# Performance work log

Hardware: AMD Instinct MI355X
Metric: run time of the kernel (lower is better)

Reference implementation:

```python
import jax, jax.numpy as jnp
import numpy as np

# distilled LLaVA-style decoder: nf4-quantized linears + LoRA(q/k/v/o) + gumbel-softmax -> embedding einsum
B, S, D, H, L = 1, 2048, 2048, 16, 2
DH = D // H
DFF, V, R, BLK = 8192, 32000, 8, 64
LORA_SCALE = 16.0 / R  # alpha / r
TAU = 1.0
SQRT_DH = float(np.sqrt(DH))

# bitsandbytes NF4 codebook (16 values)
NF4 = jnp.array([-1.0, -0.6961928009986877, -0.5250730514526367, -0.39491748809814453,
                 -0.28444138169288635, -0.18477343022823334, -0.09105003625154495, 0.0,
                 0.07958029955625534, 0.16093020141124725, 0.24611230194568634,
                 0.33791524171829224, 0.44070982933044434, 0.5626170039176941,
                 0.7229568362236023, 1.0], dtype=jnp.float32)


def dequant(idx, scale):
    # idx [..., out, in] int in [0,16); scale [..., out, in//BLK] per-block absmax
    return NF4[idx] * jnp.repeat(scale, BLK, axis=-1)


def rmsnorm(x, w):
    return x * jax.lax.rsqrt(jnp.mean(x * x, axis=-1, keepdims=True) + 1e-6) * w


def setup_inputs():
    key = jax.random.key(0)
    k = jax.random.split(key, 12)
    return {
        "input_ids": jax.random.randint(k[0], (B, S), 0, V, dtype=jnp.int32),
        "u": jax.random.uniform(k[1], (B, S, V), dtype=jnp.float32),
        "emb": jax.random.normal(k[2], (V, D), dtype=jnp.float32) * 0.02,
        "attn_scale": jax.random.uniform(k[3], (L, 4, D, D // BLK), minval=0.005, maxval=0.02, dtype=jnp.float32),
        "ffn_gu_scale": jax.random.uniform(k[4], (L, 2, DFF, D // BLK), minval=0.005, maxval=0.02, dtype=jnp.float32),
        "ffn_d_scale": jax.random.uniform(k[5], (L, D, DFF // BLK), minval=0.005, maxval=0.02, dtype=jnp.float32),
        "lora_A": jax.random.normal(k[6], (L, 4, R, D), dtype=jnp.float32) * 0.01,
        "lora_B": jax.random.normal(k[7], (L, 4, D, R), dtype=jnp.float32) * 0.01,
        "norm_w": jnp.ones((L, 2, D), dtype=jnp.float32),
        "final_norm_w": jnp.ones((D,), dtype=jnp.float32),
        "attn_idx": jax.random.randint(k[8], (L, 4, D, D), 0, 16, dtype=jnp.int32),
        "ffn_gu_idx": jax.random.randint(k[9], (L, 2, DFF, D), 0, 16, dtype=jnp.int32),
        "ffn_d_idx": jax.random.randint(k[10], (L, D, DFF), 0, 16, dtype=jnp.int32),
    }


def reference(input_ids, u, emb, attn_scale, ffn_gu_scale, ffn_d_scale,
              lora_A, lora_B, norm_w, final_norm_w, attn_idx, ffn_gu_idx, ffn_d_idx):
    h = emb[input_ids]  # [B, S, D]
    causal = jnp.tril(jnp.ones((S, S), dtype=bool))
    for l in range(L):
        x = rmsnorm(h, norm_w[l, 0])
        w = dequant(attn_idx[l], attn_scale[l])  # [4, D, D] dequantized q/k/v/o weights

        def proj(i, t):
            # nf4 linear + LoRA adapter (y = t W^T + (t A^T) B^T * alpha/r)
            return t @ w[i].T + ((t @ lora_A[l, i].T) @ lora_B[l, i].T) * LORA_SCALE

        q = proj(0, x).reshape(B, S, H, DH)
        k_ = proj(1, x).reshape(B, S, H, DH)
        v = proj(2, x).reshape(B, S, H, DH)
        scores = jnp.einsum('bqhd,bkhd->bhqk', q, k_) / SQRT_DH
        scores = jnp.where(causal, scores, -1e30)
        p = jax.nn.softmax(scores, axis=-1)
        o = jnp.einsum('bhqk,bkhd->bqhd', p, v).reshape(B, S, D)
        h = h + proj(3, o)

        x = rmsnorm(h, norm_w[l, 1])
        wgu = dequant(ffn_gu_idx[l], ffn_gu_scale[l])  # [2, DFF, D] gate/up
        wd = dequant(ffn_d_idx[l], ffn_d_scale[l])     # [D, DFF] down
        h = h + (jax.nn.silu(x @ wgu[0].T) * (x @ wgu[1].T)) @ wd.T

    h = rmsnorm(h, final_norm_w)
    logits = h @ emb.T  # [B, S, V]
    # gumbel_softmax(tau, hard=False): softmax((logits + G)/tau), G = -log(-log(U))
    gnoise = -jnp.log(-jnp.log(u + 1e-10) + 1e-10)
    g = jax.nn.softmax((logits + gnoise) / TAU, axis=-1)
    soft_embeddings = jnp.einsum('bsv,vd->bsd', g, emb)
    return soft_embeddings, logits
```

## Files before the change

kernel.cpp:

```cpp
#include <hip/hip_runtime.h>
#include <hip/hip_bf16.h>

typedef unsigned short u16;
typedef unsigned int u32;
typedef __bf16 bf16t;
typedef bf16t bf16x8 __attribute__((ext_vector_type(8)));
typedef float f32x4 __attribute__((ext_vector_type(4)));

constexpr int S_   = 2048;
constexpr int D_   = 2048;
constexpr int H_   = 16;
constexpr int DH_  = 128;
constexpr int L_   = 2;
constexpr int DFF_ = 8192;
constexpr int V_   = 32000;
constexpr int R_   = 8;

#define MFMA16(a, b, c) __builtin_amdgcn_mfma_f32_16x16x32_bf16(a, b, c, 0, 0, 0)

__constant__ float c_nf4[16] = {
  -1.0f, -0.6961928009986877f, -0.5250730514526367f, -0.39491748809814453f,
  -0.28444138169288635f, -0.18477343022823334f, -0.09105003625154495f, 0.0f,
  0.07958029955625534f, 0.16093020141124725f, 0.24611230194568634f,
  0.33791524171829224f, 0.44070982933044434f, 0.5626170039176941f,
  0.7229568362236023f, 1.0f };

__device__ __forceinline__ u16 f2bf(float f) {
  union { float f; u32 u; } v; v.f = f;
  u32 r = v.u + 0x7fffu + ((v.u >> 16) & 1u);
  return (u16)(r >> 16);
}
__device__ __forceinline__ float bf2f(u16 h) {
  union { u32 u; float f; } v; v.u = ((u32)h) << 16; return v.f;
}

__global__ __launch_bounds__(256) void k_gather(const int* __restrict__ ids,
                                                const float* __restrict__ emb,
                                                float* __restrict__ h) {
  int t = blockIdx.x * 256 + threadIdx.x;
  int s = t >> 11;
  int d = t & 2047;
  h[t] = emb[(size_t)ids[s] * D_ + d];
}

__global__ __launch_bounds__(256) void k_rmsnorm(const float* __restrict__ in,
                                                 const float* __restrict__ w,
                                                 u16* __restrict__ out) {
  int s = blockIdx.x;
  const float* x = in + (size_t)s * D_;
  float ss = 0.f;
  for (int d = threadIdx.x; d < D_; d += 256) { float v = x[d]; ss += v * v; }
#pragma unroll
  for (int m = 1; m < 64; m <<= 1) ss += __shfl_xor(ss, m, 64);
  __shared__ float sh[4];
  if ((threadIdx.x & 63) == 0) sh[threadIdx.x >> 6] = ss;
  __syncthreads();
  ss = sh[0] + sh[1] + sh[2] + sh[3];
  float sc = rsqrtf(ss * (1.0f / D_) + 1e-6f);
  u16* o = out + (size_t)s * D_;
  for (int d = threadIdx.x; d < D_; d += 256) o[d] = f2bf(x[d] * sc * w[d]);
}

__global__ __launch_bounds__(256) void k_dequant(const int* __restrict__ idx,
                                                 const float* __restrict__ scale,
                                                 u16* __restrict__ out, int kshift) {
  size_t t = (size_t)blockIdx.x * 256 + threadIdx.x;
  size_t e = t * 8;
  int k = (int)(e & ((1u << kshift) - 1));
  size_t n = e >> kshift;
  float s = scale[(n << (kshift - 6)) + (k >> 6)];
  int4 i0 = *(const int4*)(idx + e);
  int4 i1 = *(const int4*)(idx + e + 4);
  uint4 o;
  o.x = (u32)f2bf(c_nf4[i0.x] * s) | ((u32)f2bf(c_nf4[i0.y] * s) << 16);
  o.y = (u32)f2bf(c_nf4[i0.z] * s) | ((u32)f2bf(c_nf4[i0.w] * s) << 16);
  o.z = (u32)f2bf(c_nf4[i1.x] * s) | ((u32)f2bf(c_nf4[i1.y] * s) << 16);
  o.w = (u32)f2bf(c_nf4[i1.z] * s) | ((u32)f2bf(c_nf4[i1.w] * s) << 16);
  *(uint4*)(out + e) = o;
}

__global__ __launch_bounds__(256) void k_embprep(const float* __restrict__ src,
                                                 u16* __restrict__ embb,
                                                 u16* __restrict__ embT) {
  __shared__ u16 tile[64][65];
  int v0 = blockIdx.x * 64, d0 = blockIdx.y * 64;
  int tid = threadIdx.x;
  int rr = tid >> 4, cc = (tid & 15) * 4;
#pragma unroll
  for (int j = 0; j < 4; ++j) {
    int r = j * 16 + rr;
    float4 f = *(const float4*)(src + (size_t)(v0 + r) * D_ + d0 + cc);
    u16 b0 = f2bf(f.x), b1 = f2bf(f.y), b2 = f2bf(f.z), b3 = f2bf(f.w);
    tile[r][cc + 0] = b0; tile[r][cc + 1] = b1;
    tile[r][cc + 2] = b2; tile[r][cc + 3] = b3;
    ushort4 wv; wv.x = b0; wv.y = b1; wv.z = b2; wv.w = b3;
    *(ushort4*)(embb + (size_t)(v0 + r) * D_ + d0 + cc) = wv;
  }
  __syncthreads();
#pragma unroll
  for (int j = 0; j < 4; ++j) {
    int r = j * 16 + rr;
    ushort4 w;
    w.x = tile[cc + 0][r]; w.y = tile[cc + 1][r];
    w.z = tile[cc + 2][r]; w.w = tile[cc + 3][r];
    *(ushort4*)(embT + (size_t)(d0 + r) * V_ + v0 + cc) = w;
  }
}

enum { OUT_F32 = 0, OUT_F32_ACC = 1, OUT_BF16 = 2 };

template<int OUTMODE>
__global__ __launch_bounds__(512, 2) void k_gemm256(const u16* __restrict__ A, int lda,
                                                    const u16* __restrict__ B, int ldb,
                                                    void* __restrict__ Cv, int ldc,
                                                    int Kc, size_t zstride) {
  __shared__ u16 As[2][256][64];
  __shared__ u16 Bs[2][256][64];
  const int tid = threadIdx.x;
  const int lane = tid & 63, w = tid >> 6;
  const int wr = w >> 2, wc = w & 3;
  const int g = (lane >> 4), l15 = lane & 15, sl7 = lane & 7;

  const int gx = gridDim.x, gy = gridDim.y;
  const int cpx = (gx * gy) >> 3;
  int d = blockIdx.y * gx + blockIdx.x;
  int swz = (d & 7) * cpx + (d >> 3);
  const int m0 = (swz % gy) * 256;
  const int n0 = (swz / gy) * 256;

  A += (size_t)blockIdx.z * Kc;
  B += (size_t)blockIdx.z * Kc;
  float* Cf = (float*)Cv + (size_t)blockIdx.z * zstride;

  const int NT = Kc >> 6;
  const int srow = w * 8 + (lane >> 3);
  const int sch  = (lane & 7) ^ (lane >> 3);

  auto stageA = [&](int half, int tile) {
    const u16* src = A + (size_t)(m0 + half * 128 + srow) * lda + tile * 64 + sch * 8;
    u16* dst = &As[tile & 1][half * 128 + w * 8][0];
#pragma unroll
    for (int rnd = 0; rnd < 2; ++rnd)
      __builtin_amdgcn_global_load_lds(
          (const __attribute__((address_space(1))) void*)(src + (size_t)rnd * 64 * lda),
          (__attribute__((address_space(3))) void*)(dst + rnd * 64 * 64), 16, 0, 0);
  };
  auto stageB = [&](int half, int tile) {
    const u16* src = B + (size_t)(n0 + half * 128 + srow) * ldb + tile * 64 + sch * 8;
    u16* dst = &Bs[tile & 1][half * 128 + w * 8][0];
#pragma unroll
    for (int rnd = 0; rnd < 2; ++rnd)
      __builtin_amdgcn_global_load_lds(
          (const __attribute__((address_space(1))) void*)(src + (size_t)rnd * 64 * ldb),
          (__attribute__((address_space(3))) void*)(dst + rnd * 64 * 64), 16, 0, 0);
  };

  f32x4 acc[8][4] = {};
  bf16x8 areg[4][2], breg[2][2][2];

  stageB(0, 0); stageB(1, 0); stageA(0, 0); stageA(1, 0);
  if (NT > 1) {
    stageB(0, 1); stageB(1, 1); stageA(0, 1); stageA(1, 1);
    asm volatile("s_waitcnt vmcnt(8)" ::: "memory");
  } else {
    asm volatile("s_waitcnt vmcnt(0)" ::: "memory");
  }
  __builtin_amdgcn_s_barrier();

#define LOADA(QR)                                                                   \
  _Pragma("unroll") for (int m = 0; m < 4; ++m)                                     \
    _Pragma("unroll") for (int kh = 0; kh < 2; ++kh) {                              \
      int hr = wr * 128 + (QR) * 64 + m * 16 + l15;                                 \
      areg[m][kh] = *(const bf16x8*)(abase + hr * 64 + ((((kh << 2) | g) ^ sl7) << 3)); \
    }
#define LOADB(QC)                                                                   \
  _Pragma("unroll") for (int n = 0; n < 2; ++n)                                     \
    _Pragma("unroll") for (int kh = 0; kh < 2; ++kh) {                              \
      int br = wc * 64 + (QC) * 32 + n * 16 + l15;                                  \
      breg[QC][n][kh] = *(const bf16x8*)(bbase + br * 64 + ((((kh << 2) | g) ^ sl7) << 3)); \
    }
#define QPHASE(QR, QC)                                                              \
  __builtin_amdgcn_s_setprio(1);                                                    \
  _Pragma("unroll") for (int m = 0; m < 4; ++m)                                     \
    _Pragma("unroll") for (int n = 0; n < 2; ++n)                                   \
      _Pragma("unroll") for (int kh = 0; kh < 2; ++kh)                              \
        acc[(QR) * 4 + m][(QC) * 2 + n] = __builtin_amdgcn_mfma_f32_16x16x32_bf16(  \
            areg[m][kh], breg[QC][n][kh], acc[(QR) * 4 + m][(QC) * 2 + n], 0, 0, 0); \
  __builtin_amdgcn_s_setprio(0);

  for (int t = 0; t < NT; ++t) {
    const u16* abase = &As[t & 1][0][0];
    const u16* bbase = &Bs[t & 1][0][0];
    LOADA(0); LOADB(0);
    __builtin_amdgcn_s_barrier();
    asm volatile("s_waitcnt lgkmcnt(0)" ::: "memory");
    QPHASE(0, 0);
    __builtin_amdgcn_s_barrier();
    LOADB(1);
    __builtin_amdgcn_s_barrier();
    asm volatile("s_waitcnt lgkmcnt(0)" ::: "memory");
    QPHASE(0, 1);
    __builtin_amdgcn_s_barrier();
    LOADA(1);
    if (t + 2 < NT) { stageB(0, t + 2); stageB(1, t + 2); }
    __builtin_amdgcn_s_barrier();
    asm volatile("s_waitcnt lgkmcnt(0)" ::: "memory");
    QPHASE(1, 1);
    __builtin_amdgcn_s_barrier();
    if (t + 2 < NT) { stageA(0, t + 2); stageA(1, t + 2); }
    QPHASE(1, 0);
    if (t + 1 < NT) {
      if (t + 2 < NT) asm volatile("s_waitcnt vmcnt(8)" ::: "memory");
      else            asm volatile("s_waitcnt vmcnt(0)" ::: "memory");
    }
    __builtin_amdgcn_s_barrier();
  }
#undef LOADA
#undef LOADB
#undef QPHASE

  const int er = g * 4;
#pragma unroll
  for (int i = 0; i < 8; ++i)
#pragma unroll
    for (int j = 0; j < 4; ++j)
#pragma unroll
      for (int r = 0; r < 4; ++r) {
        int row = m0 + wr * 128 + i * 16 + er + r;
        int col = n0 + wc * 64 + j * 16 + l15;
        if (OUTMODE == OUT_BF16) {
          ((u16*)Cv)[(size_t)row * ldc + col] = f2bf(acc[i][j][r]);
        } else if (OUTMODE == OUT_F32_ACC) {
          Cf[(size_t)row * ldc + col] += acc[i][j][r];
        } else {
          Cf[(size_t)row * ldc + col] = acc[i][j][r];
        }
      }
}

__global__ __launch_bounds__(256) void k_red(const float* __restrict__ P,
                                             float* __restrict__ dst, int accmode) {
  size_t i = ((size_t)blockIdx.x * 256 + threadIdx.x) * 4;
  const size_t n = (size_t)4 * 1024 * 1024;
  float4 a = *(const float4*)(P + i);
  float4 b = *(const float4*)(P + n + i);
  float4 c = *(const float4*)(P + 2 * n + i);
  float4 d = *(const float4*)(P + 3 * n + i);
  float4 r;
  r.x = (a.x + b.x) + (c.x + d.x);
  r.y = (a.y + b.y) + (c.y + d.y);
  r.z = (a.z + b.z) + (c.z + d.z);
  r.w = (a.w + b.w) + (c.w + d.w);
  if (accmode) {
    float4 o = *(const float4*)(dst + i);
    r.x += o.x; r.y += o.y; r.z += o.z; r.w += o.w;
  }
  *(float4*)(dst + i) = r;
}

__global__ __launch_bounds__(256) void k_lora_down(const u16* __restrict__ X,
                                                   const float* __restrict__ A,
                                                   float* __restrict__ T, int nproj) {
  int s = blockIdx.x;
  int lane = threadIdx.x & 63, wv = threadIdx.x >> 6;
  const u16* x = X + (size_t)s * D_;
  for (int p = wv; p < nproj * R_; p += 4) {
    const float* a = A + (size_t)p * D_;
    float sum = 0.f;
    for (int d = lane; d < D_; d += 64) sum += bf2f(x[d]) * a[d];
#pragma unroll
    for (int m = 1; m < 64; m <<= 1) sum += __shfl_xor(sum, m, 64);
    if (lane == 0) T[(size_t)s * (nproj * R_) + p] = sum;
  }
}

__global__ __launch_bounds__(256) void k_lora_up(float* __restrict__ Y, int ystride,
                                                 const float* __restrict__ T,
                                                 const float* __restrict__ Bm, int nproj) {
  int t = blockIdx.x * 256 + threadIdx.x;
  int d = t & (D_ - 1);
  int si = t >> 11;
  int i = si % nproj;
  int s = si / nproj;
  const float* tp = T + ((size_t)s * nproj + i) * R_;
  const float* bp = Bm + ((size_t)i * D_ + d) * R_;
  float acc = 0.f;
#pragma unroll
  for (int r = 0; r < R_; r++) acc += tp[r] * bp[r];
  Y[(size_t)s * ystride + (size_t)i * D_ + d] += 2.0f * acc;
}

__global__ __launch_bounds__(256) void k_lora_up_qkv(u16* __restrict__ qkvb,
                                                     const float* __restrict__ T,
                                                     const float* __restrict__ Bm) {
  size_t t = ((size_t)blockIdx.x * 256 + threadIdx.x) * 8;
  int c = (int)(t % 6144);
  int s = (int)(t / 6144);
  int i = c >> 11, dd = c & 2047;
  const float* tp = T + ((size_t)s * 3 + i) * R_;
  float tr[8];
#pragma unroll
  for (int r = 0; r < R_; ++r) tr[r] = tp[r];
  uint4 q = *(const uint4*)(qkvb + t);
  u16 qs[8] = {(u16)(q.x & 0xffff), (u16)(q.x >> 16), (u16)(q.y & 0xffff), (u16)(q.y >> 16),
               (u16)(q.z & 0xffff), (u16)(q.z >> 16), (u16)(q.w & 0xffff), (u16)(q.w >> 16)};
  u16 os[8];
#pragma unroll
  for (int j = 0; j < 8; ++j) {
    const float* bp = Bm + ((size_t)i * D_ + dd + j) * R_;
    float a = 0.f;
#pragma unroll
    for (int r = 0; r < R_; ++r) a += tr[r] * bp[r];
    os[j] = f2bf(bf2f(qs[j]) + 2.0f * a);
  }
  uint4 o;
  o.x = (u32)os[0] | ((u32)os[1] << 16);
  o.y = (u32)os[2] | ((u32)os[3] << 16);
  o.z = (u32)os[4] | ((u32)os[5] << 16);
  o.w = (u32)os[6] | ((u32)os[7] << 16);
  *(uint4*)(qkvb + t) = o;
}

__global__ __launch_bounds__(256) void k_vtrans(const u16* __restrict__ qkvb,
                                                u16* __restrict__ Vt) {
  __shared__ u16 t[64][136];
  int s0 = blockIdx.x * 64, hh = blockIdx.y;
  int tid = threadIdx.x;
#pragma unroll
  for (int it = 0; it < 4; ++it) {
    int e = it * 2048 + tid * 8;
    int sr = e >> 7, sc = e & 127;
    *(uint4*)&t[sr][sc] =
        *(const uint4*)(qkvb + (size_t)(s0 + sr) * 6144 + 4096 + hh * 128 + sc);
  }
  __syncthreads();
#pragma unroll
  for (int it = 0; it < 4; ++it) {
    int q = it * 256 + tid;
    int dh = q >> 3, sc = (q & 7) * 8;
    u16 e0 = t[sc + 0][dh], e1 = t[sc + 1][dh], e2 = t[sc + 2][dh], e3 = t[sc + 3][dh];
    u16 e4 = t[sc + 4][dh], e5 = t[sc + 5][dh], e6 = t[sc + 6][dh], e7 = t[sc + 7][dh];
    uint4 o;
    o.x = (u32)e0 | ((u32)e1 << 16);
    o.y = (u32)e2 | ((u32)e3 << 16);
    o.z = (u32)e4 | ((u32)e5 << 16);
    o.w = (u32)e6 | ((u32)e7 << 16);
    *(uint4*)(Vt + ((size_t)hh * DH_ + dh) * S_ + s0 + sc) = o;
  }
}

__global__ __launch_bounds__(256) void k_attn2(const u16* __restrict__ qkvb,
                                               const u16* __restrict__ Vt,
                                               u16* __restrict__ out) {
  __shared__ u16 Ks[2][64 * 128];
  __shared__ u16 VTs[2][128 * 64];
  __shared__ u16 PT[4][64 * 16];
  const int tid = threadIdx.x;
  const int lane = tid & 63, w = tid >> 6;
  const int g = lane >> 4, l4 = lane & 15;
  const int p = blockIdx.x;
  const int hh = blockIdx.y;
  const int ld = 6144;
  const float rs = 0.08838834764831845f;
  const int qa0 = p * 64, qb0 = (31 - p) * 64;
  const int ntb = 32 - p;
  char* pt_w = (char*)&PT[w][0];

  const int qga = qa0 + w * 16 + l4;
  const int qgb = qb0 + w * 16 + l4;

  bf16x8 qfa[4], qfb[4];
#pragma unroll
  for (int kh = 0; kh < 4; ++kh) {
    qfa[kh] = *(const bf16x8*)(qkvb + (size_t)qga * ld + hh * DH_ + kh * 32 + g * 8);
    qfb[kh] = *(const bf16x8*)(qkvb + (size_t)qgb * ld + hh * DH_ + kh * 32 + g * 8);
  }

  float ma = -3.0e38f, la = 0.f, mb = -3.0e38f, lb = 0.f;
  f32x4 acc_a[8] = {}, acc_b[8] = {};
  bf16x8 pba[2], pbb[2];

  auto stage = [&](int buf, int kt) {
    const int kv0 = kt * 64;
#pragma unroll
    for (int i = 0; i < 4; ++i) {
      int rl = (w * 4 + i) * 4 + (lane >> 4);
      int cs = (lane & 15) ^ ((rl & 7) ^ (((rl >> 3) & 3) << 1));
      __builtin_amdgcn_global_load_lds(
          (const __attribute__((address_space(1))) void*)(
              qkvb + (size_t)(kv0 + rl) * ld + 2048 + hh * DH_ + cs * 8),
          (__attribute__((address_space(3))) void*)(&Ks[buf][(w * 4 + i) * 512]), 16, 0, 0);
    }
#pragma unroll
    for (int i = 0; i < 4; ++i) {
      int dh = (w * 4 + i) * 8 + (lane >> 3);
      int cs = (lane & 7) ^ (dh & 7);
      __builtin_amdgcn_global_load_lds(
          (const __attribute__((address_space(1))) void*)(
              Vt + ((size_t)hh * DH_ + dh) * S_ + kv0 + cs * 8),
          (__attribute__((address_space(3))) void*)(&VTs[buf][(w * 4 + i) * 512]), 16, 0, 0);
    }
  };

  auto softpb = [&](f32x4* sv, float& m, float& l, f32x4* acc, int qg, bool diag,
                    int kv0, bf16x8* pb) {
    float pv[16];
    float tmax = -3.0e38f;
#pragma unroll
    for (int kb = 0; kb < 4; ++kb)
#pragma unroll
      for (int r = 0; r < 4; ++r) {
        float s = sv[kb][r] * rs;
        if (diag) {
          int kglob = kv0 + kb * 16 + g * 4 + r;
          if (kglob > qg) s = -1.0e30f;
        }
        pv[kb * 4 + r] = s;
        tmax = fmaxf(tmax, s);
      }
    tmax = fmaxf(tmax, __shfl_xor(tmax, 16, 64));
    tmax = fmaxf(tmax, __shfl_xor(tmax, 32, 64));
    float mn = fmaxf(m, tmax);
    float corr = __expf(m - mn);
    m = mn;
    float ps = 0.f;
#pragma unroll
    for (int i = 0; i < 16; ++i) { pv[i] = __expf(pv[i] - mn); ps += pv[i]; }
    ps += __shfl_xor(ps, 16, 64);
    ps += __shfl_xor(ps, 32, 64);
    l = l * corr + ps;
#pragma unroll
    for (int f = 0; f < 8; ++f) {
      acc[f][0] *= corr; acc[f][1] *= corr; acc[f][2] *= corr; acc[f][3] *= corr;
    }
#pragma unroll
    for (int kb = 0; kb < 4; ++kb)
#pragma unroll
      for (int r = 0; r < 4; ++r) {
        int key = kb * 16 + g * 4 + r;
        int byte = (key * 32 + l4 * 2) ^ (((key >> 3) & 3) << 5);
        *(u16*)(pt_w + byte) = f2bf(pv[kb * 4 + r]);
      }
#pragma unroll
    for (int ks = 0; ks < 2; ++ks) {
      union { bf16x8 v; u16 s[8]; } ub;
#pragma unroll
      for (int j = 0; j < 8; ++j) {
        int key = ks * 32 + g * 8 + j;
        int byte = (key * 32 + l4 * 2) ^ (((key >> 3) & 3) << 5);
        ub.s[j] = *(const u16*)(pt_w + byte);
      }
      pb[ks] = ub.v;
    }
  };

  stage(0, 0);
  asm volatile("s_waitcnt vmcnt(0)" ::: "memory");
  __syncthreads();

  for (int kt = 0; kt < ntb; ++kt) {
    const int kv0 = kt * 64;
    const int buf = kt & 1;
    if (kt + 1 < ntb) stage(buf ^ 1, kt + 1);

    const char* kb_base = (const char*)&Ks[buf][0];
    const char* vb_base = (const char*)&VTs[buf][0];
    const bool doa = (kt <= p);

    f32x4 sa[4] = {}, sb[4] = {};
#pragma unroll
    for (int kb = 0; kb < 4; ++kb) {
#pragma unroll
      for (int kh = 0; kh < 4; ++kh) {
        int key = kb * 16 + l4;
        int ch = (kh * 4 + g) ^ ((key & 7) ^ (((key >> 3) & 3) << 1));
        bf16x8 af = *(const bf16x8*)(kb_base + key * 256 + ch * 16);
        if (doa) sa[kb] = MFMA16(af, qfa[kh], sa[kb]);
        sb[kb] = MFMA16(af, qfb[kh], sb[kb]);
      }
    }

    if (doa) softpb(sa, ma, la, acc_a, qga, kt == p, kv0, pba);
    softpb(sb, mb, lb, acc_b, qgb, kt == ntb - 1, kv0, pbb);

#pragma unroll
    for (int f = 0; f < 8; ++f) {
#pragma unroll
      for (int ks = 0; ks < 2; ++ks) {
        int dh = f * 16 + l4;
        int ch = (ks * 4 + g) ^ (dh & 7);
        bf16x8 va = *(const bf16x8*)(vb_base + dh * 128 + ch * 16);
        if (doa) acc_a[f] = MFMA16(va, pba[ks], acc_a[f]);
        acc_b[f] = MFMA16(va, pbb[ks], acc_b[f]);
      }
    }

    if (kt + 1 < ntb) {
      asm volatile("s_waitcnt vmcnt(0)" ::: "memory");
      __syncthreads();
    }
  }

  float inva = 1.f / la, invb = 1.f / lb;
  u16* opa = out + (size_t)qga * D_ + hh * DH_;
  u16* opb = out + (size_t)qgb * D_ + hh * DH_;
#pragma unroll
  for (int f = 0; f < 8; ++f)
#pragma unroll
    for (int r = 0; r < 4; ++r) {
      opa[f * 16 + g * 4 + r] = f2bf(acc_a[f][r] * inva);
      opb[f * 16 + g * 4 + r] = f2bf(acc_b[f][r] * invb);
    }
}

__global__ __launch_bounds__(256) void k_silumul(u16* __restrict__ gu) {
  size_t i = ((size_t)blockIdx.x * 256 + threadIdx.x) * 4;
  int s = (int)(i >> 13);
  int f = (int)(i & 8191);
  u16* gp = gu + (size_t)s * (2 * DFF_) + f;
  ushort4 gt = *(ushort4*)gp;
  ushort4 up = *(ushort4*)(gp + DFF_);
  float g0 = bf2f(gt.x), g1 = bf2f(gt.y), g2 = bf2f(gt.z), g3 = bf2f(gt.w);
  float u0 = bf2f(up.x), u1 = bf2f(up.y), u2 = bf2f(up.z), u3 = bf2f(up.w);
  ushort4 o;
  o.x = f2bf(g0 / (1.f + __expf(-g0)) * u0);
  o.y = f2bf(g1 / (1.f + __expf(-g1)) * u1);
  o.z = f2bf(g2 / (1.f + __expf(-g2)) * u2);
  o.w = f2bf(g3 / (1.f + __expf(-g3)) * u3);
  *(ushort4*)gp = o;
}

__global__ __launch_bounds__(256) void k_gumbel(const float* __restrict__ logits,
                                                const float* __restrict__ u,
                                                u16* __restrict__ g) {
  __shared__ float z[V_];
  __shared__ float sred[4];
  int s = blockIdx.x;
  const float* lp = logits + (size_t)s * V_;
  const float* up = u + (size_t)s * V_;
  float m = -3.0e38f;
  for (int v4 = threadIdx.x; v4 < V_ / 4; v4 += 256) {
    float4 lv = *(const float4*)(lp + v4 * 4);
    float4 uv = *(const float4*)(up + v4 * 4);
    float z0 = lv.x - __logf(-__logf(uv.x + 1e-10f) + 1e-10f);
    float z1 = lv.y - __logf(-__logf(uv.y + 1e-10f) + 1e-10f);
    float z2 = lv.z - __logf(-__logf(uv.z + 1e-10f) + 1e-10f);
    float z3 = lv.w - __logf(-__logf(uv.w + 1e-10f) + 1e-10f);
    *(float4*)(z + v4 * 4) = make_float4(z0, z1, z2, z3);
    m = fmaxf(fmaxf(fmaxf(m, z0), fmaxf(z1, z2)), z3);
  }
#pragma unroll
  for (int msk = 1; msk < 64; msk <<= 1) m = fmaxf(m, __shfl_xor(m, msk, 64));
  if ((threadIdx.x & 63) == 0) sred[threadIdx.x >> 6] = m;
  __syncthreads();
  float M = fmaxf(fmaxf(sred[0], sred[1]), fmaxf(sred[2], sred[3]));
  float l = 0.f;
  for (int v4 = threadIdx.x; v4 < V_ / 4; v4 += 256) {
    float4 zv = *(float4*)(z + v4 * 4);
    zv.x = __expf(zv.x - M); zv.y = __expf(zv.y - M);
    zv.z = __expf(zv.z - M); zv.w = __expf(zv.w - M);
    *(float4*)(z + v4 * 4) = zv;
    l += (zv.x + zv.y) + (zv.z + zv.w);
  }
#pragma unroll
  for (int msk = 1; msk < 64; msk <<= 1) l += __shfl_xor(l, msk, 64);
  __syncthreads();
  if ((threadIdx.x & 63) == 0) sred[threadIdx.x >> 6] = l;
  __syncthreads();
  float inv = 1.f / (sred[0] + sred[1] + sred[2] + sred[3]);
  u16* gp = g + (size_t)s * V_;
  for (int v4 = threadIdx.x; v4 < V_ / 4; v4 += 256) {
    float4 zv = *(float4*)(z + v4 * 4);
    ushort4 o;
    o.x = f2bf(zv.x * inv); o.y = f2bf(zv.y * inv);
    o.z = f2bf(zv.z * inv); o.w = f2bf(zv.w * inv);
    *(ushort4*)(gp + v4 * 4) = o;
  }
}

extern "C" void kernel_launch(void* const* d_in, const int* in_sizes, int n_in,
                              void* d_out, int out_size, void* d_ws, size_t ws_size,
                              hipStream_t stream) {
  const int*   ids        = (const int*)d_in[0];
  const float* u          = (const float*)d_in[1];
  const float* emb        = (const float*)d_in[2];
  const float* attn_scale = (const float*)d_in[3];
  const float* gu_scale   = (const float*)d_in[4];
  const float* dn_scale   = (const float*)d_in[5];
  const float* lora_A     = (const float*)d_in[6];
  const float* lora_B     = (const float*)d_in[7];
  const float* norm_w     = (const float*)d_in[8];
  const float* fnorm_w    = (const float*)d_in[9];
  const int*   attn_idx   = (const int*)d_in[10];
  const int*   gu_idx     = (const int*)d_in[11];
  const int*   dn_idx     = (const int*)d_in[12];

  float* out_se = (float*)d_out;
  float* out_lg = (float*)d_out + (size_t)S_ * D_;

  char* W = (char*)d_ws;
  float* h    = (float*)(W);
  u16*   xb   = (u16*)(W + ((size_t)16 << 20));
  u16*   qkvb = (u16*)(W + ((size_t)72 << 20));
  u16*   Vtb  = (u16*)(W + ((size_t)96 << 20));
  u16*   ob   = (u16*)(W + ((size_t)104 << 20));
  u16*   gub  = (u16*)(W + ((size_t)112 << 20));
  u16*   wdq  = (u16*)(W + ((size_t)176 << 20));
  float* Tl   = (float*)(W + ((size_t)240 << 20));
  u16*   embb = (u16*)(W);
  u16*   gsm  = (u16*)(W);
  u16*   embT = (u16*)(W + ((size_t)125 << 20));
  u16*   xbh  = (u16*)d_out;
  float* Pk   = (float*)(W + ((size_t)250 << 20));
  const bool big = ws_size >= ((size_t)314 << 20);
  const size_t ZS = (size_t)4 * 1024 * 1024;

  dim3 b256(256), b512(512);

  k_gather<<<dim3(S_ * D_ / 256), b256, 0, stream>>>(ids, emb, h);

  for (int l = 0; l < L_; ++l) {
    const int*   aidx = attn_idx + (size_t)l * 4 * D_ * D_;
    const float* ascl = attn_scale + (size_t)l * 4 * D_ * (D_ / 64);
    const float* lA   = lora_A + (size_t)l * 4 * R_ * D_;
    const float* lB   = lora_B + (size_t)l * 4 * D_ * R_;

    k_rmsnorm<<<dim3(S_), b256, 0, stream>>>(h, norm_w + (size_t)l * 2 * D_, xb);
    k_dequant<<<dim3(4 * D_ * D_ / 8 / 256), b256, 0, stream>>>(aidx, ascl, wdq, 11);
    k_gemm256<OUT_BF16><<<dim3(3 * D_ / 256, 8), b512, 0, stream>>>(
        xb, D_, wdq, D_, qkvb, 3 * D_, D_, 0);
    k_lora_down<<<dim3(S_), b256, 0, stream>>>(xb, lA, Tl, 3);
    k_lora_up_qkv<<<dim3(S_ * 3 * D_ / 8 / 256), b256, 0, stream>>>(qkvb, Tl, lB);
    k_vtrans<<<dim3(S_ / 64, H_), b256, 0, stream>>>(qkvb, Vtb);
    k_attn2<<<dim3(16, H_), b256, 0, stream>>>(qkvb, Vtb, ob);
    if (big) {
      k_gemm256<OUT_F32><<<dim3(D_ / 256, 8, 4), b512, 0, stream>>>(
          ob, D_, wdq + (size_t)3 * D_ * D_, D_, Pk, D_, D_ / 4, ZS);
      k_red<<<dim3(4096), b256, 0, stream>>>(Pk, h, 1);
    } else {
      k_gemm256<OUT_F32_ACC><<<dim3(D_ / 256, 8), b512, 0, stream>>>(
          ob, D_, wdq + (size_t)3 * D_ * D_, D_, h, D_, D_, 0);
    }
    k_lora_down<<<dim3(S_), b256, 0, stream>>>(ob, lA + (size_t)3 * R_ * D_, Tl, 1);
    k_lora_up<<<dim3(S_ * D_ / 256), b256, 0, stream>>>(h, D_, Tl, lB + (size_t)3 * D_ * R_, 1);

    k_rmsnorm<<<dim3(S_), b256, 0, stream>>>(h, norm_w + (size_t)l * 2 * D_ + D_, xb);
    k_dequant<<<dim3(2 * DFF_ * D_ / 8 / 256), b256, 0, stream>>>(
        gu_idx + (size_t)l * 2 * DFF_ * D_, gu_scale + (size_t)l * 2 * DFF_ * (D_ / 64), wdq, 11);
    k_gemm256<OUT_BF16><<<dim3(2 * DFF_ / 256, 8), b512, 0, stream>>>(
        xb, D_, wdq, D_, gub, 2 * DFF_, D_, 0);
    k_silumul<<<dim3(S_ * DFF_ / 4 / 256), b256, 0, stream>>>(gub);
    k_dequant<<<dim3(D_ * DFF_ / 8 / 256), b256, 0, stream>>>(
        dn_idx + (size_t)l * D_ * DFF_, dn_scale + (size_t)l * D_ * (DFF_ / 64), wdq, 13);
    if (big) {
      k_gemm256<OUT_F32><<<dim3(D_ / 256, 8, 4), b512, 0, stream>>>(
          gub, 2 * DFF_, wdq, DFF_, Pk, D_, DFF_ / 4, ZS);
      k_red<<<dim3(4096), b256, 0, stream>>>(Pk, h, 1);
    } else {
      k_gemm256<OUT_F32_ACC><<<dim3(D_ / 256, 8), b512, 0, stream>>>(
          gub, 2 * DFF_, wdq, DFF_, h, D_, DFF_, 0);
    }
  }

  k_rmsnorm<<<dim3(S_), b256, 0, stream>>>(h, fnorm_w, xbh);
  k_embprep<<<dim3(V_ / 64, D_ / 64), b256, 0, stream>>>(emb, embb, embT);
  k_gemm256<OUT_F32><<<dim3(V_ / 256, 8), b512, 0, stream>>>(
      xbh, D_, embb, D_, out_lg, V_, D_, 0);
  k_gumbel<<<dim3(S_), b256, 0, stream>>>(out_lg, u, gsm);
  if (big) {
    k_gemm256<OUT_F32><<<dim3(D_ / 256, 8, 4), b512, 0, stream>>>(
        gsm, V_, embT, V_, Pk, D_, V_ / 4, ZS);
    k_red<<<dim3(4096), b256, 0, stream>>>(Pk, out_se, 0);
  } else {
    k_gemm256<OUT_F32><<<dim3(D_ / 256, 8), b512, 0, stream>>>(
        gsm, V_, embT, V_, out_se, D_, V_, 0);
  }
}
```

Measured before the change: 2.346 ms.

## Split attention KV loop across two blocks and merge partials with rescaling

Causal attention now runs a split-KV (flash-decoding style) scheme. Each (pair, head) block is split in two along the key axis with interleaved tiles, and each half writes normalized partial outputs plus running max and sum. A new reduction kernel merges the two halves with log-sum-exp weighting. This doubles the grid from 256 to 512 blocks to fill more CUs, in exchange for an extra kernel launch, extra global traffic for the partial outputs, and bf16 rounding of the partials.

```diff
diff --git a/kernel.cpp b/kernel.cpp
--- a/kernel.cpp
+++ b/kernel.cpp
@@ -349,9 +349,10 @@
   }
 }
 
-__global__ __launch_bounds__(256) void k_attn2(const u16* __restrict__ qkvb,
+__global__ __launch_bounds__(256) void k_attn3(const u16* __restrict__ qkvb,
                                                const u16* __restrict__ Vt,
-                                               u16* __restrict__ out) {
+                                               u16* __restrict__ Op,
+                                               float2* __restrict__ st) {
   __shared__ u16 Ks[2][64 * 128];
   __shared__ u16 VTs[2][128 * 64];
   __shared__ u16 PT[4][64 * 16];
@@ -360,6 +361,7 @@
   const int g = lane >> 4, l4 = lane & 15;
   const int p = blockIdx.x;
   const int hh = blockIdx.y;
+  const int z = blockIdx.z;
   const int ld = 6144;
   const float rs = 0.08838834764831845f;
   const int qa0 = p * 64, qb0 = (31 - p) * 64;
@@ -454,14 +456,15 @@
     }
   };
 
-  stage(0, 0);
+  stage(0, z);
   asm volatile("s_waitcnt vmcnt(0)" ::: "memory");
   __syncthreads();
 
-  for (int kt = 0; kt < ntb; ++kt) {
+  int it = 0;
+  for (int kt = z; kt < ntb; kt += 2, ++it) {
     const int kv0 = kt * 64;
-    const int buf = kt & 1;
-    if (kt + 1 < ntb) stage(buf ^ 1, kt + 1);
+    const int buf = it & 1;
+    if (kt + 2 < ntb) stage(buf ^ 1, kt + 2);
 
     const char* kb_base = (const char*)&Ks[buf][0];
     const char* vb_base = (const char*)&VTs[buf][0];
@@ -495,15 +498,16 @@
       }
     }
 
-    if (kt + 1 < ntb) {
+    if (kt + 2 < ntb) {
       asm volatile("s_waitcnt vmcnt(0)" ::: "memory");
       __syncthreads();
     }
   }
 
-  float inva = 1.f / la, invb = 1.f / lb;
-  u16* opa = out + (size_t)qga * D_ + hh * DH_;
-  u16* opb = out + (size_t)qgb * D_ + hh * DH_;
+  float inva = la > 0.f ? 1.f / la : 0.f;
+  float invb = lb > 0.f ? 1.f / lb : 0.f;
+  u16* opa = Op + (size_t)z * S_ * D_ + (size_t)qga * D_ + hh * DH_;
+  u16* opb = Op + (size_t)z * S_ * D_ + (size_t)qgb * D_ + hh * DH_;
 #pragma unroll
   for (int f = 0; f < 8; ++f)
 #pragma unroll
@@ -511,6 +515,45 @@
       opa[f * 16 + g * 4 + r] = f2bf(acc_a[f][r] * inva);
       opb[f * 16 + g * 4 + r] = f2bf(acc_b[f][r] * invb);
     }
+  if (g == 0) {
+    float2 va; va.x = ma; va.y = la;
+    float2 vb; vb.x = mb; vb.y = lb;
+    st[(size_t)z * S_ * H_ + (size_t)qga * H_ + hh] = va;
+    st[(size_t)z * S_ * H_ + (size_t)qgb * H_ + hh] = vb;
+  }
+}
+
+__global__ __launch_bounds__(256) void k_attnred(const u16* __restrict__ Op,
+                                                 const float2* __restrict__ st,
+                                                 u16* __restrict__ out) {
+  size_t t = (size_t)blockIdx.x * 256 + threadIdx.x;
+  int dh8 = (int)(t & 15);
+  int sh  = (int)(t >> 4);
+  float2 s0 = st[sh];
+  float2 s1 = st[(size_t)S_ * H_ + sh];
+  float M = fmaxf(s0.x, s1.x);
+  float w0 = s0.y * __expf(s0.x - M);
+  float w1 = s1.y * __expf(s1.x - M);
+  float inv = 1.f / (w0 + w1);
+  w0 *= inv; w1 *= inv;
+  int h = sh & 15, s = sh >> 4;
+  size_t off = (size_t)s * D_ + (size_t)h * DH_ + (size_t)dh8 * 8;
+  uint4 a = *(const uint4*)(Op + off);
+  uint4 b = *(const uint4*)(Op + (size_t)S_ * D_ + off);
+  u16 av[8] = {(u16)(a.x & 0xffff), (u16)(a.x >> 16), (u16)(a.y & 0xffff), (u16)(a.y >> 16),
+               (u16)(a.z & 0xffff), (u16)(a.z >> 16), (u16)(a.w & 0xffff), (u16)(a.w >> 16)};
+  u16 bv[8] = {(u16)(b.x & 0xffff), (u16)(b.x >> 16), (u16)(b.y & 0xffff), (u16)(b.y >> 16),
+               (u16)(b.z & 0xffff), (u16)(b.z >> 16), (u16)(b.w & 0xffff), (u16)(b.w >> 16)};
+  u16 ov[8];
+#pragma unroll
+  for (int j = 0; j < 8; ++j)
+    ov[j] = f2bf(w0 * bf2f(av[j]) + w1 * bf2f(bv[j]));
+  uint4 o;
+  o.x = (u32)ov[0] | ((u32)ov[1] << 16);
+  o.y = (u32)ov[2] | ((u32)ov[3] << 16);
+  o.z = (u32)ov[4] | ((u32)ov[5] << 16);
+  o.w = (u32)ov[6] | ((u32)ov[7] << 16);
+  *(uint4*)(out + off) = o;
 }
 
 __global__ __launch_bounds__(256) void k_silumul(u16* __restrict__ gu) {
@@ -605,6 +648,8 @@
   u16*   Vtb  = (u16*)(W + ((size_t)96 << 20));
   u16*   ob   = (u16*)(W + ((size_t)104 << 20));
   u16*   gub  = (u16*)(W + ((size_t)112 << 20));
+  u16*    apart = (u16*)(W + ((size_t)112 << 20));
+  float2* astat = (float2*)(W + ((size_t)128 << 20));
   u16*   wdq  = (u16*)(W + ((size_t)176 << 20));
   float* Tl   = (float*)(W + ((size_t)240 << 20));
   u16*   embb = (u16*)(W);
@@ -632,7 +677,8 @@
     k_lora_down<<<dim3(S_), b256, 0, stream>>>(xb, lA, Tl, 3);
     k_lora_up_qkv<<<dim3(S_ * 3 * D_ / 8 / 256), b256, 0, stream>>>(qkvb, Tl, lB);
     k_vtrans<<<dim3(S_ / 64, H_), b256, 0, stream>>>(qkvb, Vtb);
-    k_attn2<<<dim3(16, H_), b256, 0, stream>>>(qkvb, Vtb, ob);
+    k_attn3<<<dim3(16, H_, 2), b256, 0, stream>>>(qkvb, Vtb, apart, astat);
+    k_attnred<<<dim3(S_ * H_ * 16 / 256), b256, 0, stream>>>(apart, astat, ob);
     if (big) {
       k_gemm256<OUT_F32><<<dim3(D_ / 256, 8, 4), b512, 0, stream>>>(
           ob, D_, wdq + (size_t)3 * D_ * D_, D_, Pk, D_, D_ / 4, ZS);
```

After: 2.337 ms. No clear change (-0.4%).
